# Optimization experiments

Hardware: AMD Instinct MI355X
Metric: run time of the kernel (lower is better)

Reference implementation:

```python
import jax, jax.numpy as jnp
import numpy as np

GRAPH_SIZE = 512  # N: graph_size from init


def setup_inputs() -> dict:
    key = jax.random.key(0)
    k1, k2 = jax.random.split(key)
    B, N, C_IN, C_OUT = 128, GRAPH_SIZE, 128, 128
    # X packs [adjacency | features] along last dim, matching the torch forward
    X = jax.random.uniform(k1, (B, N, N + C_IN), dtype=jnp.float32)
    W = jax.random.normal(k2, (C_IN, C_OUT), dtype=jnp.float32)
    return {"X": X, "W": W}


def reference(X, W):
    N = GRAPH_SIZE
    A = X[:, :, :N]            # [B, N, N] dense adjacency
    feat = X[:, :, N:]         # [B, N, C_in]
    # D = diag(rowsum(A)); pinv(D).sqrt() == diag(1/sqrt(deg)) with 0 where deg==0
    deg = jnp.sum(A, axis=2)   # [B, N]
    d_inv_sqrt = jnp.where(deg > 0, 1.0 / jnp.sqrt(deg), 0.0)
    A_hat = A + jnp.eye(N, dtype=A.dtype)  # A + I
    # D^-1/2 @ A_hat @ D^-1/2 as elementwise row/col scaling (diag matmuls)
    A_norm = d_inv_sqrt[:, :, None] * A_hat * d_inv_sqrt[:, None, :]
    # relu(A_norm @ X @ W)
    h = jnp.einsum('bnm,bmf->bnf', A_norm, feat)
    out = jax.nn.relu(jnp.einsum('bnf,fo->bno', h, W))
    return jnp.concatenate([A, out], axis=2)  # [B, N, N + C_out]
```

## Files before the change

kernel.cpp:

```cpp
#include <hip/hip_runtime.h>
#include <stdint.h>

#define GS   512
#define CF   128
#define XROW 640
#define NB   128

typedef __attribute__((ext_vector_type(4))) float          f32x4;
typedef __attribute__((ext_vector_type(2))) float          f32x2;
typedef __attribute__((ext_vector_type(8))) short          s16x8;
typedef __attribute__((ext_vector_type(4))) unsigned short u16x4;
typedef __attribute__((ext_vector_type(8))) unsigned short u16x8;

__device__ __forceinline__ unsigned short f2bf(float f) {
    unsigned u = __builtin_bit_cast(unsigned, f);
    u = (u + 0x7fffu + ((u >> 16) & 1u)) >> 16;
    return (unsigned short)u;
}
__device__ __forceinline__ float bf2f(unsigned short h) {
    unsigned u = ((unsigned)h) << 16;
    return __builtin_bit_cast(float, u);
}
__device__ __forceinline__ void glds16(const void* g, void* l) {
    __builtin_amdgcn_global_load_lds(
        (const __attribute__((address_space(1))) void*)g,
        (__attribute__((address_space(3))) void*)l, 16, 0, 0);
}

__global__ __launch_bounds__(256) void k0_wt(const float* __restrict__ W,
                                             unsigned short* __restrict__ WTst) {
    const int e = blockIdx.x * 256 + threadIdx.x;
    const int j = e & 7, f = (e >> 3) & 127, q = e >> 10;
    const int c = (q >> 2) * 32 + (q & 3) * 8 + j;
    WTst[e] = f2bf(W[c * CF + f]);
}

__global__ __launch_bounds__(256, 4) void k12(const float* __restrict__ X,
                                              const unsigned short* __restrict__ WTst,
                                              float* __restrict__ out,
                                              float* __restrict__ dis,
                                              unsigned short* __restrict__ Abf,
                                              unsigned short* __restrict__ fwdT) {
    __shared__ __align__(16) unsigned short sfb[64 * 128];
    __shared__ __align__(16) float spart[64 * 16];
    __shared__ __align__(16) float sdis[64];
    const int t = threadIdx.x, l = t & 63, wv = t >> 6;
    const int m0 = blockIdx.x << 6;
    const int b = m0 >> 9, ml0 = m0 & (GS - 1);

    for (int p = 0; p < 16; ++p) {
        const int rw = (p << 2) + wv;
        const int gr = m0 + rw;
        const float* row = X + (size_t)gr * XROW;
        const f32x4* rp = (const f32x4*)row;
        f32x4 v0 = rp[2 * l], v1 = rp[2 * l + 1];
        f32x2 vf = *(const f32x2*)(row + GS + 2 * l);
        f32x4* op = (f32x4*)(out + (size_t)gr * XROW);
        op[2 * l] = v0; op[2 * l + 1] = v1;
        u16x8 o;
        o[0] = f2bf(v0[0]); o[1] = f2bf(v0[1]); o[2] = f2bf(v0[2]); o[3] = f2bf(v0[3]);
        o[4] = f2bf(v1[0]); o[5] = f2bf(v1[1]); o[6] = f2bf(v1[2]); o[7] = f2bf(v1[3]);
        *(u16x8*)((char*)Abf + ((size_t)gr << 10) + (l << 4)) = o;
        unsigned fo = (unsigned)f2bf(vf[0]) | ((unsigned)f2bf(vf[1]) << 16);
        int ad = (rw << 8) + (l << 2);
        ad ^= (rw & 7) << 4;
        *(unsigned*)((char*)sfb + ad) = fo;
        float s = (v0[0] + v0[1]) + (v0[2] + v0[3]) + (v1[0] + v1[1]) + (v1[2] + v1[3]);
        s += __shfl_xor(s, 32);
        s += __shfl_xor(s, 16);
        if (l < 16) spart[(rw << 4) + l] = s;
    }
    __syncthreads();

    {
        const int r = t >> 2, c = t & 3;
        f32x4 pv = *(const f32x4*)&spart[(r << 4) + (c << 2)];
        float s = (pv[0] + pv[1]) + (pv[2] + pv[3]);
        s += __shfl_xor(s, 1);
        s += __shfl_xor(s, 2);
        if (c == 0) {
            float d = (s > 0.f) ? (1.f / sqrtf(s)) : 0.f;
            sdis[r] = d; dis[m0 + r] = d;
        }
    }
    __syncthreads();

    const int wr = wv >> 1, wc = wv & 1, lr = l & 15, lk = l >> 4;
    f32x4 acc[2][4];
#pragma unroll
    for (int i = 0; i < 2; ++i)
#pragma unroll
        for (int j = 0; j < 4; ++j)
#pragma unroll
            for (int r = 0; r < 4; ++r) acc[i][j][r] = 0.f;

#pragma unroll
    for (int ks = 0; ks < 4; ++ks) {
        s16x8 af[2];
#pragma unroll
        for (int i = 0; i < 2; ++i) {
            int row = (wr << 5) + (i << 4) + lr;
            int ad = (row << 8) + (((ks << 2) | lk) << 4);
            ad ^= (row & 7) << 4;
            af[i] = *(const s16x8*)((char*)sfb + ad);
        }
#pragma unroll
        for (int j = 0; j < 4; ++j) {
            int f = (wc << 6) + (j << 4) + lr;
            s16x8 bfr = *(const s16x8*)(WTst + (((((ks << 2) | lk) << 7) | f) << 3));
#pragma unroll
            for (int i = 0; i < 2; ++i)
                acc[i][j] = __builtin_amdgcn_mfma_f32_16x16x32_bf16(af[i], bfr, acc[i][j], 0, 0, 0);
        }
    }

#pragma unroll
    for (int i = 0; i < 2; ++i) {
        int mr = (wr << 5) + (i << 4) + (lk << 2);
        f32x4 d4 = *(const f32x4*)&sdis[mr];
        int mg = ml0 + mr;
        int ktm = mg >> 5, q3 = (mg >> 3) & 3, jm = mg & 7;
#pragma unroll
        for (int j = 0; j < 4; ++j) {
            int f = (wc << 6) + (j << 4) + lr;
            u16x4 o;
            o[0] = f2bf(d4[0] * acc[i][j][0]);
            o[1] = f2bf(d4[1] * acc[i][j][1]);
            o[2] = f2bf(d4[2] * acc[i][j][2]);
            o[3] = f2bf(d4[3] * acc[i][j][3]);
            *(u16x4*)((char*)fwdT + ((size_t)b << 17) + (((ktm << 2) | q3) << 11)
                      + (f << 4) + (jm << 1)) = o;
        }
    }
}

__global__ __launch_bounds__(256) void k3_gcn(const unsigned short* __restrict__ Abf,
                                              const float* __restrict__ dis,
                                              const unsigned short* __restrict__ fwdT,
                                              float* __restrict__ out) {
    __shared__ __align__(16) unsigned short sb[2][8192];
    const int t = threadIdx.x, l = t & 63, wv = t >> 6, lr = l & 15, lk = l >> 4;
    const int ord = blockIdx.x;
    const int L = ((ord & 7) << 7) + (ord >> 3);
    const int b = L >> 3, bm0 = (L & 7) << 6;
    const char* Bt = (const char*)fwdT + ((size_t)b << 17);
    const char* Ab = (const char*)Abf
        + (((size_t)(b * GS + bm0 + (wv << 4) + lr)) << 10) + (lk << 4);

    auto stage = [&](int buf, int ph) {
#pragma unroll
        for (int it = 0; it < 4; ++it)
            glds16(Bt + (ph << 14) + it * 4096 + wv * 1024 + l * 16,
                   (char*)sb[buf] + it * 4096 + wv * 1024);
    };

    f32x4 acc[8];
#pragma unroll
    for (int j = 0; j < 8; ++j)
#pragma unroll
        for (int r = 0; r < 4; ++r) acc[j][r] = 0.f;

    stage(0, 0);
    s16x8 a0 = *(const s16x8*)(Ab);
    s16x8 a1 = *(const s16x8*)(Ab + 64);
    int cur = 0;
    for (int ph = 0; ph < 8; ++ph) {
        __syncthreads();
        if (ph < 7) stage(cur ^ 1, ph + 1);
        s16x8 n0 = a0, n1 = a1;
        if (ph < 7) {
            n0 = *(const s16x8*)(Ab + ((2 * ph + 2) << 6));
            n1 = *(const s16x8*)(Ab + ((2 * ph + 3) << 6));
        }
#pragma unroll
        for (int j = 0; j < 8; ++j) {
            s16x8 bfr = *(const s16x8*)&sb[cur][(lk << 10) + (j << 7) + (lr << 3)];
            acc[j] = __builtin_amdgcn_mfma_f32_16x16x32_bf16(a0, bfr, acc[j], 0, 0, 0);
        }
#pragma unroll
        for (int j = 0; j < 8; ++j) {
            s16x8 bfr = *(const s16x8*)&sb[cur][4096 + (lk << 10) + (j << 7) + (lr << 3)];
            acc[j] = __builtin_amdgcn_mfma_f32_16x16x32_bf16(a1, bfr, acc[j], 0, 0, 0);
        }
        a0 = n0; a1 = n1; cur ^= 1;
    }

    const int n0r = bm0 + (wv << 4) + (lk << 2);
    f32x4 d4 = *(const f32x4*)&dis[(b << 9) + n0r];
    const int ktm = n0r >> 5, q3 = (n0r >> 3) & 3, jm = n0r & 7;
#pragma unroll
    for (int j = 0; j < 8; ++j) {
        int f = (j << 4) + lr;
        u16x4 fw = *(const u16x4*)(Bt + (((ktm << 2) | q3) << 11) + (f << 4) + (jm << 1));
        float* ob = out + ((size_t)(b * GS + n0r)) * XROW + GS + f;
#pragma unroll
        for (int r = 0; r < 4; ++r) {
            float v = d4[r] * (acc[j][r] + bf2f(fw[r]));
            ob[(size_t)r * XROW] = v > 0.f ? v : 0.f;
        }
    }
}

extern "C" void kernel_launch(void* const* d_in, const int* in_sizes, int n_in,
                              void* d_out, int out_size, void* d_ws, size_t ws_size,
                              hipStream_t stream) {
    const float* X = (const float*)d_in[0];
    const float* W = (const float*)d_in[1];
    float* out = (float*)d_out;
    float*          dis  = (float*)d_ws;
    unsigned short* WTst = (unsigned short*)((char*)d_ws + 262144);
    unsigned short* fwdT = (unsigned short*)((char*)d_ws + 294912);
    unsigned short* Abf  = (unsigned short*)((char*)d_ws + 17072128);

    hipLaunchKernelGGL(k0_wt, dim3(64),            dim3(256), 0, stream, W, WTst);
    hipLaunchKernelGGL(k12,   dim3(NB * GS / 64),  dim3(256), 0, stream, X, WTst, out, dis, Abf, fwdT);
    hipLaunchKernelGGL(k3_gcn, dim3(NB * GS / 64), dim3(256), 0, stream, Abf, dis, fwdT, out);
}
```

Baseline: 335.4 us.

## Drop bf16 adjacency copy; read fp32 X directly in GEMM with packed converts

Removes the intermediate bf16 adjacency buffer. The aggregation GEMM now loads fp32 adjacency rows straight from X and converts them with v_cvt_pk_bf16_f32. The fused stage is split into a degree/copy kernel and a feature-transform kernel that reads features from global memory directly. This saves writing and re-reading a 64MB bf16 buffer, but doubles the bytes the GEMM reads for A, re-reads X, and adds a kernel launch.

```diff
diff --git a/kernel.cpp b/kernel.cpp
--- a/kernel.cpp
+++ b/kernel.cpp
@@ -7,10 +7,9 @@
 #define NB   128
 
 typedef __attribute__((ext_vector_type(4))) float          f32x4;
-typedef __attribute__((ext_vector_type(2))) float          f32x2;
 typedef __attribute__((ext_vector_type(8))) short          s16x8;
 typedef __attribute__((ext_vector_type(4))) unsigned short u16x4;
-typedef __attribute__((ext_vector_type(8))) unsigned short u16x8;
+typedef __attribute__((ext_vector_type(4))) unsigned int   u32x4;
 
 __device__ __forceinline__ unsigned short f2bf(float f) {
     unsigned u = __builtin_bit_cast(unsigned, f);
@@ -21,71 +20,67 @@
     unsigned u = ((unsigned)h) << 16;
     return __builtin_bit_cast(float, u);
 }
+__device__ __forceinline__ unsigned cvtpk(float lo, float hi) {
+    unsigned r;
+    asm volatile("v_cvt_pk_bf16_f32 %0, %1, %2" : "=v"(r) : "v"(lo), "v"(hi));
+    return r;
+}
+__device__ __forceinline__ s16x8 pack8(f32x4 x0, f32x4 x1) {
+    u32x4 p;
+    p[0] = cvtpk(x0[0], x0[1]); p[1] = cvtpk(x0[2], x0[3]);
+    p[2] = cvtpk(x1[0], x1[1]); p[3] = cvtpk(x1[2], x1[3]);
+    return __builtin_bit_cast(s16x8, p);
+}
 __device__ __forceinline__ void glds16(const void* g, void* l) {
     __builtin_amdgcn_global_load_lds(
         (const __attribute__((address_space(1))) void*)g,
         (__attribute__((address_space(3))) void*)l, 16, 0, 0);
 }
 
-__global__ __launch_bounds__(256) void k0_wt(const float* __restrict__ W,
-                                             unsigned short* __restrict__ WTst) {
+__global__ __launch_bounds__(256) void k0_wt2(const float* __restrict__ W,
+                                              unsigned short* __restrict__ WTst) {
     const int e = blockIdx.x * 256 + threadIdx.x;
-    const int j = e & 7, f = (e >> 3) & 127, q = e >> 10;
+    const int f = (e >> 3) & 127, q = e >> 10, j = e & 7;
     const int c = (q >> 2) * 32 + (q & 3) * 8 + j;
     WTst[e] = f2bf(W[c * CF + f]);
 }
 
-__global__ __launch_bounds__(256, 4) void k12(const float* __restrict__ X,
-                                              const unsigned short* __restrict__ WTst,
-                                              float* __restrict__ out,
-                                              float* __restrict__ dis,
-                                              unsigned short* __restrict__ Abf,
-                                              unsigned short* __restrict__ fwdT) {
-    __shared__ __align__(16) unsigned short sfb[64 * 128];
-    __shared__ __align__(16) float spart[64 * 16];
-    __shared__ __align__(16) float sdis[64];
+__global__ __launch_bounds__(256) void kD(const float* __restrict__ X,
+                                          float* __restrict__ out,
+                                          float* __restrict__ dis) {
+    __shared__ float spart[64 * 68];
+    const int t = threadIdx.x, l = t & 63, wv = t >> 6;
+    const int m0 = blockIdx.x << 6;
+    for (int p = 0; p < 16; ++p) {
+        const int rw = (p << 2) + wv, gr = m0 + rw;
+        const f32x4* rp = (const f32x4*)(X + (size_t)gr * XROW);
+        f32x4* op = (f32x4*)(out + (size_t)gr * XROW);
+        f32x4 v0 = rp[l], v1 = rp[l + 64];
+        op[l] = v0; op[l + 64] = v1;
+        spart[rw * 68 + l] = (v0[0] + v0[1]) + (v0[2] + v0[3])
+                           + (v1[0] + v1[1]) + (v1[2] + v1[3]);
+    }
+    __syncthreads();
+    const int r = t >> 2, c = t & 3;
+    const float* pr = &spart[r * 68 + (c << 4)];
+    f32x4 a0 = *(const f32x4*)pr,       a1 = *(const f32x4*)(pr + 4);
+    f32x4 a2 = *(const f32x4*)(pr + 8), a3 = *(const f32x4*)(pr + 12);
+    float s = ((a0[0] + a0[1]) + (a0[2] + a0[3])) + ((a1[0] + a1[1]) + (a1[2] + a1[3]))
+            + ((a2[0] + a2[1]) + (a2[2] + a2[3])) + ((a3[0] + a3[1]) + (a3[2] + a3[3]));
+    s += __shfl_xor(s, 1);
+    s += __shfl_xor(s, 2);
+    if (c == 0) dis[m0 + r] = (s > 0.f) ? (1.f / sqrtf(s)) : 0.f;
+}
+
+__global__ __launch_bounds__(256) void kPre(const float* __restrict__ X,
+                                            const unsigned short* __restrict__ WTst,
+                                            const float* __restrict__ dis,
+                                            unsigned short* __restrict__ fwdT) {
     const int t = threadIdx.x, l = t & 63, wv = t >> 6;
     const int m0 = blockIdx.x << 6;
     const int b = m0 >> 9, ml0 = m0 & (GS - 1);
-
-    for (int p = 0; p < 16; ++p) {
-        const int rw = (p << 2) + wv;
-        const int gr = m0 + rw;
-        const float* row = X + (size_t)gr * XROW;
-        const f32x4* rp = (const f32x4*)row;
-        f32x4 v0 = rp[2 * l], v1 = rp[2 * l + 1];
-        f32x2 vf = *(const f32x2*)(row + GS + 2 * l);
-        f32x4* op = (f32x4*)(out + (size_t)gr * XROW);
-        op[2 * l] = v0; op[2 * l + 1] = v1;
-        u16x8 o;
-        o[0] = f2bf(v0[0]); o[1] = f2bf(v0[1]); o[2] = f2bf(v0[2]); o[3] = f2bf(v0[3]);
-        o[4] = f2bf(v1[0]); o[5] = f2bf(v1[1]); o[6] = f2bf(v1[2]); o[7] = f2bf(v1[3]);
-        *(u16x8*)((char*)Abf + ((size_t)gr << 10) + (l << 4)) = o;
-        unsigned fo = (unsigned)f2bf(vf[0]) | ((unsigned)f2bf(vf[1]) << 16);
-        int ad = (rw << 8) + (l << 2);
-        ad ^= (rw & 7) << 4;
-        *(unsigned*)((char*)sfb + ad) = fo;
-        float s = (v0[0] + v0[1]) + (v0[2] + v0[3]) + (v1[0] + v1[1]) + (v1[2] + v1[3]);
-        s += __shfl_xor(s, 32);
-        s += __shfl_xor(s, 16);
-        if (l < 16) spart[(rw << 4) + l] = s;
-    }
-    __syncthreads();
-
-    {
-        const int r = t >> 2, c = t & 3;
-        f32x4 pv = *(const f32x4*)&spart[(r << 4) + (c << 2)];
-        float s = (pv[0] + pv[1]) + (pv[2] + pv[3]);
-        s += __shfl_xor(s, 1);
-        s += __shfl_xor(s, 2);
-        if (c == 0) {
-            float d = (s > 0.f) ? (1.f / sqrtf(s)) : 0.f;
-            sdis[r] = d; dis[m0 + r] = d;
-        }
-    }
-    __syncthreads();
-
     const int wr = wv >> 1, wc = wv & 1, lr = l & 15, lk = l >> 4;
+
     f32x4 acc[2][4];
 #pragma unroll
     for (int i = 0; i < 2; ++i)
@@ -99,10 +94,10 @@
         s16x8 af[2];
 #pragma unroll
         for (int i = 0; i < 2; ++i) {
-            int row = (wr << 5) + (i << 4) + lr;
-            int ad = (row << 8) + (((ks << 2) | lk) << 4);
-            ad ^= (row & 7) << 4;
-            af[i] = *(const s16x8*)((char*)sfb + ad);
+            int row = m0 + (wr << 5) + (i << 4) + lr;
+            const float* fp = X + (size_t)row * XROW + GS + (ks << 5) + (lk << 3);
+            f32x4 x0 = *(const f32x4*)fp, x1 = *(const f32x4*)(fp + 4);
+            af[i] = pack8(x0, x1);
         }
 #pragma unroll
         for (int j = 0; j < 4; ++j) {
@@ -117,7 +112,7 @@
 #pragma unroll
     for (int i = 0; i < 2; ++i) {
         int mr = (wr << 5) + (i << 4) + (lk << 2);
-        f32x4 d4 = *(const f32x4*)&sdis[mr];
+        f32x4 d4 = *(const f32x4*)&dis[m0 + mr];
         int mg = ml0 + mr;
         int ktm = mg >> 5, q3 = (mg >> 3) & 3, jm = mg & 7;
 #pragma unroll
@@ -134,7 +129,7 @@
     }
 }
 
-__global__ __launch_bounds__(256) void k3_gcn(const unsigned short* __restrict__ Abf,
+__global__ __launch_bounds__(256) void k3_gcn(const float* __restrict__ X,
                                               const float* __restrict__ dis,
                                               const unsigned short* __restrict__ fwdT,
                                               float* __restrict__ out) {
@@ -144,8 +139,7 @@
     const int L = ((ord & 7) << 7) + (ord >> 3);
     const int b = L >> 3, bm0 = (L & 7) << 6;
     const char* Bt = (const char*)fwdT + ((size_t)b << 17);
-    const char* Ab = (const char*)Abf
-        + (((size_t)(b * GS + bm0 + (wv << 4) + lr)) << 10) + (lk << 4);
+    const float* Arow = X + (size_t)(b * GS + bm0 + (wv << 4) + lr) * XROW + (lk << 3);
 
     auto stage = [&](int buf, int ph) {
 #pragma unroll
@@ -161,17 +155,19 @@
         for (int r = 0; r < 4; ++r) acc[j][r] = 0.f;
 
     stage(0, 0);
-    s16x8 a0 = *(const s16x8*)(Ab);
-    s16x8 a1 = *(const s16x8*)(Ab + 64);
+    f32x4 a00 = *(const f32x4*)(Arow),      a01 = *(const f32x4*)(Arow + 4);
+    f32x4 a10 = *(const f32x4*)(Arow + 32), a11 = *(const f32x4*)(Arow + 36);
     int cur = 0;
     for (int ph = 0; ph < 8; ++ph) {
         __syncthreads();
         if (ph < 7) stage(cur ^ 1, ph + 1);
-        s16x8 n0 = a0, n1 = a1;
+        f32x4 n00 = a00, n01 = a01, n10 = a10, n11 = a11;
         if (ph < 7) {
-            n0 = *(const s16x8*)(Ab + ((2 * ph + 2) << 6));
-            n1 = *(const s16x8*)(Ab + ((2 * ph + 3) << 6));
-        }
+            const float* nA = Arow + ((2 * ph + 2) << 5);
+            n00 = *(const f32x4*)(nA);      n01 = *(const f32x4*)(nA + 4);
+            n10 = *(const f32x4*)(nA + 32); n11 = *(const f32x4*)(nA + 36);
+        }
+        s16x8 a0 = pack8(a00, a01), a1 = pack8(a10, a11);
 #pragma unroll
         for (int j = 0; j < 8; ++j) {
             s16x8 bfr = *(const s16x8*)&sb[cur][(lk << 10) + (j << 7) + (lr << 3)];
@@ -182,7 +178,7 @@
             s16x8 bfr = *(const s16x8*)&sb[cur][4096 + (lk << 10) + (j << 7) + (lr << 3)];
             acc[j] = __builtin_amdgcn_mfma_f32_16x16x32_bf16(a1, bfr, acc[j], 0, 0, 0);
         }
-        a0 = n0; a1 = n1; cur ^= 1;
+        a00 = n00; a01 = n01; a10 = n10; a11 = n11; cur ^= 1;
     }
 
     const int n0r = bm0 + (wv << 4) + (lk << 2);
@@ -210,9 +206,9 @@
     float*          dis  = (float*)d_ws;
     unsigned short* WTst = (unsigned short*)((char*)d_ws + 262144);
     unsigned short* fwdT = (unsigned short*)((char*)d_ws + 294912);
-    unsigned short* Abf  = (unsigned short*)((char*)d_ws + 17072128);
-
-    hipLaunchKernelGGL(k0_wt, dim3(64),            dim3(256), 0, stream, W, WTst);
-    hipLaunchKernelGGL(k12,   dim3(NB * GS / 64),  dim3(256), 0, stream, X, WTst, out, dis, Abf, fwdT);
-    hipLaunchKernelGGL(k3_gcn, dim3(NB * GS / 64), dim3(256), 0, stream, Abf, dis, fwdT, out);
-}
+
+    hipLaunchKernelGGL(k0_wt2, dim3(64),           dim3(256), 0, stream, W, WTst);
+    hipLaunchKernelGGL(kD,     dim3(NB * GS / 64), dim3(256), 0, stream, X, out, dis);
+    hipLaunchKernelGGL(kPre,   dim3(NB * GS / 64), dim3(256), 0, stream, X, WTst, dis, fwdT);
+    hipLaunchKernelGGL(k3_gcn, dim3(NB * GS / 64), dim3(256), 0, stream, X, dis, fwdT, out);
+}
```

After: 337.6 us. About the same (+0.7%).
